# Kernel optimization log

Hardware: AMD Instinct MI355X
Metric: run time of the kernel (lower is better)

The kernel has to match this reference:

```python
import jax, jax.numpy as jnp
import numpy as np

B, T, C = 256, 2048, 64  # batch, max_seq_len, num_classes


def setup_inputs() -> dict:
    key = jax.random.key(0)
    k1, k2, k3, k4 = jax.random.split(key, 4)
    pad_x = jax.random.normal(k1, (B, T, C), dtype=jnp.float32)
    transitions = jax.random.uniform(k2, (C, C), dtype=jnp.float32)
    origination = jax.random.uniform(k3, (C,), dtype=jnp.float32)
    batch_sizes = jnp.sort(jax.random.randint(k4, (B,), 1, T + 1))
    # the torch implementation assumes features are zero-padded past the length
    mask = jnp.arange(T)[None, :] < batch_sizes[:, None]  # (B, T)
    pad_x = pad_x * mask[:, :, None]
    return {"pad_x": pad_x, "transitions": transitions,
            "origination": origination, "batch_sizes": batch_sizes}


def reference(pad_x, transitions, origination, batch_sizes):
    # Linear-chain CRF forward algorithm (faithful to torch _forward_algo,
    # including the final sum over classes rather than logsumexp).
    x_tbc = jnp.swapaxes(pad_x, 0, 1)  # (T, B, C)
    alpha0 = x_tbc[0] + origination[None, :]  # (B, C)

    def step(alpha_prev, x_t):
        # scores[b, j, k] = alpha_prev[b, k] + transitions[j, k]
        scores = alpha_prev[:, None, :] + transitions[None, :, :]  # (B, C, C)
        alpha = x_t + jax.nn.logsumexp(scores, axis=2)  # (B, C)
        return alpha, alpha

    _, alphas_rest = jax.lax.scan(step, alpha0, x_tbc[1:])
    alphas = jnp.concatenate([alpha0[None], alphas_rest], axis=0)  # (T, B, C)
    # gather alpha at the last valid timestep of each sequence
    final = alphas[batch_sizes - 1, jnp.arange(pad_x.shape[0])]  # (B, C)
    return final.sum(axis=1)  # (B,)
```

## Files before the change

### kernel.cpp

```cpp
#include <hip/hip_runtime.h>


#define CC 64

typedef short bf16x8 __attribute__((ext_vector_type(8)));
typedef float f32x4 __attribute__((ext_vector_type(4)));

union PackAB { int w[4]; bf16x8 v; };

__device__ __forceinline__ int cvtpk(float lo, float hi) {
    int r;
    asm("v_cvt_pk_bf16_f32 %0, %1, %2" : "=v"(r) : "v"(lo), "v"(hi));
    return r;
}
__device__ __forceinline__ float bcast0(float v) {
    return __int_as_float(__builtin_amdgcn_readfirstlane(__float_as_int(v)));
}

#define LDS_FENCE() asm volatile("s_waitcnt lgkmcnt(0)" ::: "memory")

__device__ __forceinline__ void chain_step(const bf16x8 (&A)[4][2], PackAB (&Bf)[2][4],
                                           f32x4 (&XP)[4],
                                           const float* __restrict__ xb,
                                           int tbeg, int segend, int idx, int g,
                                           float& prevS0, float& Lseg) {
    const float L2E = 1.4426950408889634f;
    float r_   = __builtin_amdgcn_rcpf(prevS0);
    float lgr_ = __builtin_amdgcn_logf(r_);
    Lseg -= lgr_;

    f32x4 exr[4];
    #pragma unroll
    for (int mt = 0; mt < 4; ++mt) {
        f32x4 xv = XP[mt];
        #pragma unroll
        for (int r = 0; r < 4; ++r)
            exr[mt][r] = __builtin_amdgcn_exp2f(fmaf(xv[r], L2E, lgr_));
    }
    {
        int tp = tbeg + 3 + idx; if (tp > segend) tp = segend;
        const float* xp = xb + (size_t)tp * CC + 4 * g;
        #pragma unroll
        for (int mt = 0; mt < 4; ++mt)
            XP[mt] = *(const f32x4*)(xp + 16 * mt);
    }

    float ns0 = 0.f;
    #pragma unroll
    for (int nt = 0; nt < 4; ++nt) {
        f32x4 Z = {0.f, 0.f, 0.f, 0.f};
        f32x4 t0, d0, d1, d2, d3;
        t0 = __builtin_amdgcn_mfma_f32_16x16x32_bf16(A[0][0], Bf[0][nt].v, Z, 0, 0, 0);
        d0 = __builtin_amdgcn_mfma_f32_16x16x32_bf16(A[0][1], Bf[1][nt].v, t0, 0, 0, 0);
        t0 = __builtin_amdgcn_mfma_f32_16x16x32_bf16(A[1][0], Bf[0][nt].v, Z, 0, 0, 0);
        d1 = __builtin_amdgcn_mfma_f32_16x16x32_bf16(A[1][1], Bf[1][nt].v, t0, 0, 0, 0);
        t0 = __builtin_amdgcn_mfma_f32_16x16x32_bf16(A[2][0], Bf[0][nt].v, Z, 0, 0, 0);
        d2 = __builtin_amdgcn_mfma_f32_16x16x32_bf16(A[2][1], Bf[1][nt].v, t0, 0, 0, 0);
        t0 = __builtin_amdgcn_mfma_f32_16x16x32_bf16(A[3][0], Bf[0][nt].v, Z, 0, 0, 0);
        d3 = __builtin_amdgcn_mfma_f32_16x16x32_bf16(A[3][1], Bf[1][nt].v, t0, 0, 0, 0);
        if (nt == 0) ns0 = d0[0];
        d0 *= exr[0]; d1 *= exr[1]; d2 *= exr[2]; d3 *= exr[3];
        Bf[0][nt].w[0] = cvtpk(d0[0], d0[1]);
        Bf[0][nt].w[1] = cvtpk(d0[2], d0[3]);
        Bf[0][nt].w[2] = cvtpk(d1[0], d1[1]);
        Bf[0][nt].w[3] = cvtpk(d1[2], d1[3]);
        Bf[1][nt].w[0] = cvtpk(d2[0], d2[1]);
        Bf[1][nt].w[1] = cvtpk(d2[2], d2[3]);
        Bf[1][nt].w[2] = cvtpk(d3[0], d3[1]);
        Bf[1][nt].w[3] = cvtpk(d3[2], d3[3]);
    }
    prevS0 = bcast0(ns0);
}

__launch_bounds__(64, 2)
__global__ void crf_seg_kernel(const float* __restrict__ x,
                               const float* __restrict__ trans,
                               const int*   __restrict__ lens,
                               unsigned short* __restrict__ Mws,
                               float* __restrict__ Ls,
                               int T, int Pseg, int Pshift, int SEG) {
    const int blk = blockIdx.x;
    const int b = blk >> Pshift;
    const int s = blk & (Pseg - 1);
    const int L = lens[b];
    const int tbeg = s * SEG;
    int segend = (s + 1) * SEG; if (segend > L - 1) segend = L - 1;
    const int nsteps = segend - tbeg;
    if (nsteps <= 0) return;

    const int l = threadIdx.x;
    const int c = l & 15, g = l >> 4;
    const float L2E = 1.4426950408889634f;
    const float* xb = x + (size_t)b * T * CC;

    bf16x8 A[4][2];
    #pragma unroll
    for (int mt = 0; mt < 4; ++mt) {
        const float* tr = trans + (16 * mt + c) * CC;
        #pragma unroll
        for (int ch = 0; ch < 2; ++ch) {
            float4 u = *(const float4*)(tr + 32 * ch + 4 * g);
            float4 v = *(const float4*)(tr + 32 * ch + 16 + 4 * g);
            PackAB pk;
            pk.w[0] = cvtpk(__builtin_amdgcn_exp2f(u.x * L2E), __builtin_amdgcn_exp2f(u.y * L2E));
            pk.w[1] = cvtpk(__builtin_amdgcn_exp2f(u.z * L2E), __builtin_amdgcn_exp2f(u.w * L2E));
            pk.w[2] = cvtpk(__builtin_amdgcn_exp2f(v.x * L2E), __builtin_amdgcn_exp2f(v.y * L2E));
            pk.w[3] = cvtpk(__builtin_amdgcn_exp2f(v.z * L2E), __builtin_amdgcn_exp2f(v.w * L2E));
            A[mt][ch] = pk.v;
        }
    }
    PackAB Bf[2][4];
    #pragma unroll
    for (int ch = 0; ch < 2; ++ch)
        #pragma unroll
        for (int nt = 0; nt < 4; ++nt)
            #pragma unroll
            for (int qq = 0; qq < 4; ++qq) {
                int i0 = 2 * qq, i1 = 2 * qq + 1;
                int k0 = 32 * ch + 4 * g + (i0 & 3) + 16 * (i0 >> 2);
                int k1 = 32 * ch + 4 * g + (i1 & 3) + 16 * (i1 >> 2);
                Bf[ch][nt].w[qq] = cvtpk((k0 == 16 * nt + c) ? 1.f : 0.f,
                                         (k1 == 16 * nt + c) ? 1.f : 0.f);
            }

    f32x4 XPa[4], XPb[4];
    {
        int t0_ = tbeg + 1;
        int t1_ = tbeg + 2; if (t1_ > segend) t1_ = segend;
        const float* xp0 = xb + (size_t)t0_ * CC + 4 * g;
        const float* xp1 = xb + (size_t)t1_ * CC + 4 * g;
        #pragma unroll
        for (int mt = 0; mt < 4; ++mt) {
            XPa[mt] = *(const f32x4*)(xp0 + 16 * mt);
            XPb[mt] = *(const f32x4*)(xp1 + 16 * mt);
        }
    }

    float Lseg = 0.f, prevS0 = 1.0f;
    int idx = 0;
    while (true) {
        chain_step(A, Bf, XPa, xb, tbeg, segend, idx, g, prevS0, Lseg);
        if (++idx >= nsteps) break;
        chain_step(A, Bf, XPb, xb, tbeg, segend, idx, g, prevS0, Lseg);
        if (++idx >= nsteps) break;
    }

    unsigned short* Mo = Mws + (size_t)blk * 4096;
    #pragma unroll
    for (int ch = 0; ch < 2; ++ch)
        #pragma unroll
        for (int nt = 0; nt < 4; ++nt)
            #pragma unroll
            for (int e = 0; e < 8; ++e) {
                unsigned wb = (unsigned)Bf[ch][nt].w[e >> 1];
                unsigned short hb = (e & 1) ? (unsigned short)(wb >> 16)
                                            : (unsigned short)(wb & 0xffffu);
                int row = 32 * ch + 4 * g + (e & 3) + 16 * (e >> 2);
                Mo[row * 64 + 16 * nt + c] = hb;
            }
    if (l == 0) Ls[blk] = Lseg;
}

__launch_bounds__(64, 1)
__global__ void crf_apply_kernel(const float* __restrict__ x,
                                 const float* __restrict__ orig,
                                 const int*   __restrict__ lens,
                                 const unsigned short* __restrict__ Mws,
                                 const float* __restrict__ Ls,
                                 float* __restrict__ out,
                                 int T, int Pseg, int SEG) {
    const int b = blockIdx.x, j = threadIdx.x;
    __shared__ float qb[CC];
    const float L2E = 1.4426950408889634f, LN2 = 0.6931471805599453f;
    const int L = lens[b];
    const float* xb = x + (size_t)b * T * CC;

    float Mbar = (xb[0] + orig[0]) * L2E;
    float q = __builtin_amdgcn_exp2f((xb[j] + orig[j]) * L2E - Mbar);

    uint4 R[8];
    {
        const uint4* Ms = (const uint4*)(Mws + ((size_t)b * Pseg + 0) * 4096 + j * 64);
        #pragma unroll
        for (int i = 0; i < 8; ++i) R[i] = Ms[i];
    }

    for (int s = 0; s < Pseg; ++s) {
        int tbeg = s * SEG;
        int segend = (s + 1) * SEG; if (segend > L - 1) segend = L - 1;
        if (segend - tbeg <= 0) break;

        uint4 Rc[8];
        #pragma unroll
        for (int i = 0; i < 8; ++i) Rc[i] = R[i];
        {
            int s2 = (s + 1 < Pseg) ? s + 1 : s;
            const uint4* Ms = (const uint4*)(Mws + ((size_t)b * Pseg + s2) * 4096 + j * 64);
            #pragma unroll
            for (int i = 0; i < 8; ++i) R[i] = Ms[i];
        }

        qb[j] = q;
        LDS_FENCE();

        float acc = 0.f;
        #pragma unroll
        for (int i = 0; i < 8; ++i) {
            f32x4 qv0 = *(const f32x4*)&qb[8 * i];
            f32x4 qv1 = *(const f32x4*)&qb[8 * i + 4];
            unsigned u0 = Rc[i].x, u1 = Rc[i].y, u2 = Rc[i].z, u3 = Rc[i].w;
            acc = fmaf(__uint_as_float(u0 << 16),        qv0[0], acc);
            acc = fmaf(__uint_as_float(u0 & 0xffff0000), qv0[1], acc);
            acc = fmaf(__uint_as_float(u1 << 16),        qv0[2], acc);
            acc = fmaf(__uint_as_float(u1 & 0xffff0000), qv0[3], acc);
            acc = fmaf(__uint_as_float(u2 << 16),        qv1[0], acc);
            acc = fmaf(__uint_as_float(u2 & 0xffff0000), qv1[1], acc);
            acc = fmaf(__uint_as_float(u3 << 16),        qv1[2], acc);
            acc = fmaf(__uint_as_float(u3 & 0xffff0000), qv1[3], acc);
        }
        float S = acc;
        Mbar += Ls[(size_t)b * Pseg + s];
        float p = bcast0(S);
        float r = __builtin_amdgcn_rcpf(p);
        float lgr = __builtin_amdgcn_logf(r);
        q = S * r;
        Mbar -= lgr;
        LDS_FENCE();
    }

    float alpha = LN2 * (Mbar + __builtin_amdgcn_logf(q));
    alpha += __shfl_xor(alpha, 1, 64);
    alpha += __shfl_xor(alpha, 2, 64);
    alpha += __shfl_xor(alpha, 4, 64);
    alpha += __shfl_xor(alpha, 8, 64);
    alpha += __shfl_xor(alpha, 16, 64);
    alpha += __shfl_xor(alpha, 32, 64);
    if (j == 0) out[b] = alpha;
}

extern "C" void kernel_launch(void* const* d_in, const int* in_sizes, int n_in,
                              void* d_out, int out_size, void* d_ws, size_t ws_size,
                              hipStream_t stream) {
    const float* x     = (const float*)d_in[0];
    const float* trans = (const float*)d_in[1];
    const float* orig  = (const float*)d_in[2];
    const int*   lens  = (const int*)d_in[3];
    float* out = (float*)d_out;

    const int B = in_sizes[3];
    const int T = in_sizes[0] / (B * CC);

    int P = 64, Pshift = 6;
    while (P > 1 && ws_size < (size_t)B * P * (4096 * 2 + 4)) { P >>= 1; --Pshift; }
    const int SEG = (T + P - 1) / P;

    unsigned short* Mws = (unsigned short*)d_ws;
    float* Ls = (float*)(Mws + (size_t)B * P * 4096);

    crf_seg_kernel<<<B * P, 64, 0, stream>>>(x, trans, lens, Mws, Ls, T, P, Pshift, SEG);
    crf_apply_kernel<<<B, 64, 0, stream>>>(x, orig, lens, Mws, Ls, out, T, P, SEG);
}
```

Before: 211.5 us.

## Pack four segment waves per block and renormalize every four chain steps

```diff
diff --git a/kernel.cpp b/kernel.cpp
--- a/kernel.cpp
+++ b/kernel.cpp
@@ -19,76 +19,27 @@
 
 #define LDS_FENCE() asm volatile("s_waitcnt lgkmcnt(0)" ::: "memory")
 
-__device__ __forceinline__ void chain_step(const bf16x8 (&A)[4][2], PackAB (&Bf)[2][4],
-                                           f32x4 (&XP)[4],
-                                           const float* __restrict__ xb,
-                                           int tbeg, int segend, int idx, int g,
-                                           float& prevS0, float& Lseg) {
-    const float L2E = 1.4426950408889634f;
-    float r_   = __builtin_amdgcn_rcpf(prevS0);
-    float lgr_ = __builtin_amdgcn_logf(r_);
-    Lseg -= lgr_;
-
-    f32x4 exr[4];
-    #pragma unroll
-    for (int mt = 0; mt < 4; ++mt) {
-        f32x4 xv = XP[mt];
-        #pragma unroll
-        for (int r = 0; r < 4; ++r)
-            exr[mt][r] = __builtin_amdgcn_exp2f(fmaf(xv[r], L2E, lgr_));
-    }
-    {
-        int tp = tbeg + 3 + idx; if (tp > segend) tp = segend;
-        const float* xp = xb + (size_t)tp * CC + 4 * g;
-        #pragma unroll
-        for (int mt = 0; mt < 4; ++mt)
-            XP[mt] = *(const f32x4*)(xp + 16 * mt);
-    }
-
-    float ns0 = 0.f;
-    #pragma unroll
-    for (int nt = 0; nt < 4; ++nt) {
-        f32x4 Z = {0.f, 0.f, 0.f, 0.f};
-        f32x4 t0, d0, d1, d2, d3;
-        t0 = __builtin_amdgcn_mfma_f32_16x16x32_bf16(A[0][0], Bf[0][nt].v, Z, 0, 0, 0);
-        d0 = __builtin_amdgcn_mfma_f32_16x16x32_bf16(A[0][1], Bf[1][nt].v, t0, 0, 0, 0);
-        t0 = __builtin_amdgcn_mfma_f32_16x16x32_bf16(A[1][0], Bf[0][nt].v, Z, 0, 0, 0);
-        d1 = __builtin_amdgcn_mfma_f32_16x16x32_bf16(A[1][1], Bf[1][nt].v, t0, 0, 0, 0);
-        t0 = __builtin_amdgcn_mfma_f32_16x16x32_bf16(A[2][0], Bf[0][nt].v, Z, 0, 0, 0);
-        d2 = __builtin_amdgcn_mfma_f32_16x16x32_bf16(A[2][1], Bf[1][nt].v, t0, 0, 0, 0);
-        t0 = __builtin_amdgcn_mfma_f32_16x16x32_bf16(A[3][0], Bf[0][nt].v, Z, 0, 0, 0);
-        d3 = __builtin_amdgcn_mfma_f32_16x16x32_bf16(A[3][1], Bf[1][nt].v, t0, 0, 0, 0);
-        if (nt == 0) ns0 = d0[0];
-        d0 *= exr[0]; d1 *= exr[1]; d2 *= exr[2]; d3 *= exr[3];
-        Bf[0][nt].w[0] = cvtpk(d0[0], d0[1]);
-        Bf[0][nt].w[1] = cvtpk(d0[2], d0[3]);
-        Bf[0][nt].w[2] = cvtpk(d1[0], d1[1]);
-        Bf[0][nt].w[3] = cvtpk(d1[2], d1[3]);
-        Bf[1][nt].w[0] = cvtpk(d2[0], d2[1]);
-        Bf[1][nt].w[1] = cvtpk(d2[2], d2[3]);
-        Bf[1][nt].w[2] = cvtpk(d3[0], d3[1]);
-        Bf[1][nt].w[3] = cvtpk(d3[2], d3[3]);
-    }
-    prevS0 = bcast0(ns0);
-}
-
-__launch_bounds__(64, 2)
+__launch_bounds__(256, 3)
 __global__ void crf_seg_kernel(const float* __restrict__ x,
                                const float* __restrict__ trans,
                                const int*   __restrict__ lens,
                                unsigned short* __restrict__ Mws,
                                float* __restrict__ Ls,
-                               int T, int Pseg, int Pshift, int SEG) {
+                               int T, int Pseg, int P4shift, int SEG) {
     const int blk = blockIdx.x;
-    const int b = blk >> Pshift;
-    const int s = blk & (Pseg - 1);
+    const int tid = threadIdx.x;
+    const int w   = tid >> 6;
+    const int l   = tid & 63;
+    const int b   = blk >> P4shift;
+    const int s   = ((blk & ((1 << P4shift) - 1)) << 2) + w;
+    if (s >= Pseg) return;
+
     const int L = lens[b];
     const int tbeg = s * SEG;
     int segend = (s + 1) * SEG; if (segend > L - 1) segend = L - 1;
     const int nsteps = segend - tbeg;
     if (nsteps <= 0) return;
 
-    const int l = threadIdx.x;
     const int c = l & 15, g = l >> 4;
     const float L2E = 1.4426950408889634f;
     const float* xb = x + (size_t)b * T * CC;
@@ -123,29 +74,85 @@
                                          (k1 == 16 * nt + c) ? 1.f : 0.f);
             }
 
-    f32x4 XPa[4], XPb[4];
+    f32x4 XPa[4], XPb[4], XPc[4], XPd[4];
     {
         int t0_ = tbeg + 1;
         int t1_ = tbeg + 2; if (t1_ > segend) t1_ = segend;
-        const float* xp0 = xb + (size_t)t0_ * CC + 4 * g;
-        const float* xp1 = xb + (size_t)t1_ * CC + 4 * g;
+        int t2_ = tbeg + 3; if (t2_ > segend) t2_ = segend;
+        int t3_ = tbeg + 4; if (t3_ > segend) t3_ = segend;
+        const float* p0 = xb + (size_t)t0_ * CC + 4 * g;
+        const float* p1 = xb + (size_t)t1_ * CC + 4 * g;
+        const float* p2 = xb + (size_t)t2_ * CC + 4 * g;
+        const float* p3 = xb + (size_t)t3_ * CC + 4 * g;
         #pragma unroll
         for (int mt = 0; mt < 4; ++mt) {
-            XPa[mt] = *(const f32x4*)(xp0 + 16 * mt);
-            XPb[mt] = *(const f32x4*)(xp1 + 16 * mt);
-        }
-    }
-
-    float Lseg = 0.f, prevS0 = 1.0f;
-    int idx = 0;
-    while (true) {
-        chain_step(A, Bf, XPa, xb, tbeg, segend, idx, g, prevS0, Lseg);
-        if (++idx >= nsteps) break;
-        chain_step(A, Bf, XPb, xb, tbeg, segend, idx, g, prevS0, Lseg);
-        if (++idx >= nsteps) break;
-    }
-
-    unsigned short* Mo = Mws + (size_t)blk * 4096;
+            XPa[mt] = *(const f32x4*)(p0 + 16 * mt);
+            XPb[mt] = *(const f32x4*)(p1 + 16 * mt);
+            XPc[mt] = *(const f32x4*)(p2 + 16 * mt);
+            XPd[mt] = *(const f32x4*)(p3 + 16 * mt);
+        }
+    }
+
+    float Lseg = 0.f;
+    float ns0  = 1.0f;
+
+    #define STEP(idx_, XP, LGR) do {                                          \
+        f32x4 exr[4];                                                         \
+        _Pragma("unroll")                                                     \
+        for (int mt = 0; mt < 4; ++mt) {                                      \
+            f32x4 xv = XP[mt];                                                \
+            _Pragma("unroll")                                                 \
+            for (int r = 0; r < 4; ++r)                                       \
+                exr[mt][r] = __builtin_amdgcn_exp2f(fmaf(xv[r], L2E, (LGR))); \
+        }                                                                     \
+        {                          \
+            int tp = tbeg + 5 + (idx_); if (tp > segend) tp = segend;         \
+            const float* xp = xb + (size_t)tp * CC + 4 * g;                   \
+            _Pragma("unroll")                                                 \
+            for (int mt = 0; mt < 4; ++mt)                                    \
+                XP[mt] = *(const f32x4*)(xp + 16 * mt);                       \
+        }                                                                     \
+        _Pragma("unroll")                                                     \
+        for (int nt = 0; nt < 4; ++nt) {                                      \
+            f32x4 Z = {0.f, 0.f, 0.f, 0.f};                                   \
+            f32x4 t0, d0, d1, d2, d3;                                         \
+            t0 = __builtin_amdgcn_mfma_f32_16x16x32_bf16(A[0][0], Bf[0][nt].v, Z, 0, 0, 0);  \
+            d0 = __builtin_amdgcn_mfma_f32_16x16x32_bf16(A[0][1], Bf[1][nt].v, t0, 0, 0, 0); \
+            t0 = __builtin_amdgcn_mfma_f32_16x16x32_bf16(A[1][0], Bf[0][nt].v, Z, 0, 0, 0);  \
+            d1 = __builtin_amdgcn_mfma_f32_16x16x32_bf16(A[1][1], Bf[1][nt].v, t0, 0, 0, 0); \
+            t0 = __builtin_amdgcn_mfma_f32_16x16x32_bf16(A[2][0], Bf[0][nt].v, Z, 0, 0, 0);  \
+            d2 = __builtin_amdgcn_mfma_f32_16x16x32_bf16(A[2][1], Bf[1][nt].v, t0, 0, 0, 0); \
+            t0 = __builtin_amdgcn_mfma_f32_16x16x32_bf16(A[3][0], Bf[0][nt].v, Z, 0, 0, 0);  \
+            d3 = __builtin_amdgcn_mfma_f32_16x16x32_bf16(A[3][1], Bf[1][nt].v, t0, 0, 0, 0); \
+            if (nt == 0) ns0 = d0[0];             \
+            d0 *= exr[0]; d1 *= exr[1]; d2 *= exr[2]; d3 *= exr[3];           \
+            Bf[0][nt].w[0] = cvtpk(d0[0], d0[1]);                             \
+            Bf[0][nt].w[1] = cvtpk(d0[2], d0[3]);                             \
+            Bf[0][nt].w[2] = cvtpk(d1[0], d1[1]);                             \
+            Bf[0][nt].w[3] = cvtpk(d1[2], d1[3]);                             \
+            Bf[1][nt].w[0] = cvtpk(d2[0], d2[1]);                             \
+            Bf[1][nt].w[1] = cvtpk(d2[2], d2[3]);                             \
+            Bf[1][nt].w[2] = cvtpk(d3[0], d3[1]);                             \
+            Bf[1][nt].w[3] = cvtpk(d3[2], d3[3]);                             \
+        }                                                                     \
+    } while (0)
+
+    for (int base = 0; base < nsteps; base += 4) {
+        float lgr = 0.f;
+        if (base > 0) {
+            float S00 = bcast0(ns0);
+            float r_  = __builtin_amdgcn_rcpf(S00);
+            lgr = __builtin_amdgcn_logf(r_);
+            Lseg -= lgr;
+        }
+        STEP(base, XPa, lgr);
+        if (base + 1 < nsteps) STEP(base + 1, XPb, 0.f);
+        if (base + 2 < nsteps) STEP(base + 2, XPc, 0.f);
+        if (base + 3 < nsteps) STEP(base + 3, XPd, 0.f);
+    }
+    #undef STEP
+
+    unsigned short* Mo = Mws + ((size_t)b * Pseg + s) * 4096;
     #pragma unroll
     for (int ch = 0; ch < 2; ++ch)
         #pragma unroll
@@ -158,7 +165,7 @@
                 int row = 32 * ch + 4 * g + (e & 3) + 16 * (e >> 2);
                 Mo[row * 64 + 16 * nt + c] = hb;
             }
-    if (l == 0) Ls[blk] = Lseg;
+    if (l == 0) Ls[(size_t)b * Pseg + s] = Lseg;
 }
 
 __launch_bounds__(64, 1)
@@ -250,13 +257,15 @@
     const int B = in_sizes[3];
     const int T = in_sizes[0] / (B * CC);
 
-    int P = 64, Pshift = 6;
-    while (P > 1 && ws_size < (size_t)B * P * (4096 * 2 + 4)) { P >>= 1; --Pshift; }
+    int P = 64;
+    while (P > 4 && ws_size < (size_t)B * P * (4096 * 2 + 4)) P >>= 1;
+    int P4shift = 0; while ((4 << P4shift) < P) ++P4shift;
     const int SEG = (T + P - 1) / P;
 
     unsigned short* Mws = (unsigned short*)d_ws;
     float* Ls = (float*)(Mws + (size_t)B * P * 4096);
 
-    crf_seg_kernel<<<B * P, 64, 0, stream>>>(x, trans, lens, Mws, Ls, T, P, Pshift, SEG);
+    crf_seg_kernel<<<B * (P >> 2), 256, 0, stream>>>(x, trans, lens, Mws, Ls,
+                                                     T, P, P4shift, SEG);
     crf_apply_kernel<<<B, 64, 0, stream>>>(x, orig, lens, Mws, Ls, out, T, P, SEG);
 }
```

After: 286.5 us. +35.5%, slower.
